# Kernel optimization log

Measured on AMD Instinct MI355X. Metric: run time of the kernel, lower is better.

Reference implementation:

```python
import jax, jax.numpy as jnp
import numpy as np

B, TD, TE, H = 8, 128, 256, 512


def setup_inputs() -> dict:
    key = jax.random.key(0)
    k1, k2, k3, k4, k5, k6 = jax.random.split(key, 6)
    enc = jax.random.normal(k1, (B, TE, H), dtype=jnp.float32)
    dec = jax.random.normal(k2, (B, TD, H), dtype=jnp.float32)
    mask = jax.random.randint(k3, (B, TE), 0, 2).astype(jnp.bool_)
    # glorot-ish scale for weights
    W1 = jax.random.normal(k4, (H, H), dtype=jnp.float32) * (1.0 / np.sqrt(H))
    W2 = jax.random.normal(k5, (H, H), dtype=jnp.float32) * (1.0 / np.sqrt(H))
    V = jax.random.normal(k6, (H, 1), dtype=jnp.float32) * (1.0 / np.sqrt(H))
    return {"encoder_outputs": enc, "decoder_outputs": dec,
            "encoder_mask": mask, "W1": W1, "W2": W2, "V": V}


def reference(encoder_outputs, decoder_outputs, encoder_mask, W1, W2, V):
    # Bahdanau additive attention.
    # enc: [B, Te, H], dec: [B, Td, H], mask: [B, Te]
    ew = jnp.einsum('bsh,hk->bsk', encoder_outputs, W1)   # [B, Te, H]
    dw = jnp.einsum('bth,hk->btk', decoder_outputs, W2)   # [B, Td, H]
    # broadcast add -> [B, Td, Te, H] (the large intermediate)
    s = jnp.tanh(ew[:, None, :, :] + dw[:, :, None, :])
    score = jnp.einsum('btsh,h->bts', s, V[:, 0])          # [B, Td, Te]
    m = encoder_mask.astype(jnp.float32)                   # [B, Te]
    score = score + (1.0 - m)[:, None, :] * (-1e9)
    attention_weights = jax.nn.softmax(score, axis=2)      # [B, Td, Te]
    context_vector = jnp.einsum('bts,bsh->bth', attention_weights, encoder_outputs)
    return context_vector, attention_weights
```

## Files before the change

### kernel.cpp

```cpp
#include <hip/hip_runtime.h>
#include <hip/hip_bf16.h>
#include <math.h>

constexpr int kB  = 8;
constexpr int kTD = 128;
constexpr int kTE = 256;
constexpr int kH  = 512;

constexpr float kTwoLog2e = 2.8853900817779268f;
constexpr float kLog2e    = 1.4426950408889634f;

constexpr int TM = 4;
constexpr int GEMM_BLOCKS = 384;

typedef __attribute__((ext_vector_type(8)))  short short8;
typedef __attribute__((ext_vector_type(16))) float f32x16;

__device__ __forceinline__ unsigned short f2bf(float x) {
    unsigned int u = __float_as_uint(x);
    return (unsigned short)((u + 0x7fffu + ((u >> 16) & 1u)) >> 16);
}
__device__ __forceinline__ float bf2f(unsigned short h) {
    return __uint_as_float(((unsigned int)h) << 16);
}

__global__ __launch_bounds__(256)
void prep_kernel(const float* __restrict__ enc, const float* __restrict__ dec,
                 const float* __restrict__ W1, const float* __restrict__ W2,
                 const void* __restrict__ mask_raw,
                 float* __restrict__ ewt, float* __restrict__ dwc,
                 float* __restrict__ mask_f) {
    const int bx = blockIdx.x;
    const int tid = threadIdx.x;

    if (bx == GEMM_BLOCKS) {
        const unsigned int* w = (const unsigned int*)mask_raw;
        unsigned int gt1 = 0, flt = 0;
        for (int i = tid; i < 512; i += 256) {
            unsigned int v = w[i];
            if (v == 0x3f800000u) flt = 1;
            else if (v > 1u) gt1 = 1;
        }
        __shared__ unsigned int s_gt1, s_flt;
        if (tid == 0) { s_gt1 = 0u; s_flt = 0u; }
        __syncthreads();
        if (gt1) atomicOr(&s_gt1, 1u);
        if (flt) atomicOr(&s_flt, 1u);
        __syncthreads();
        const int mode = s_flt ? 2 : (s_gt1 ? 1 : 0);
        for (int i = tid; i < kB * kTE; i += 256) {
            float val;
            if (mode == 2)      val = ((const float*)mask_raw)[i];
            else if (mode == 1) val = (float)(((const unsigned char*)mask_raw)[i]);
            else                val = (float)(((const int*)mask_raw)[i]);
            mask_f[i] = val;
        }
        return;
    }

    const int mt = bx >> 3;
    const int nt = bx & 7;
    const bool is_enc = (mt < 32);
    const int m0 = mt * 64;
    const int n0 = nt * 64;
    const float* Abase = is_enc ? (enc + (size_t)m0 * kH)
                                : (dec + (size_t)(m0 - 2048) * kH);
    const float* W = is_enc ? W1 : W2;

    __shared__ __align__(16) unsigned short Ahi[64][40], Alo[64][40];
    __shared__ __align__(16) unsigned short Bhi[64][40], Blo[64][40];
    __shared__ float Ws[32][68];

    const int lane = tid & 63;
    const int wv   = tid >> 6;
    const int wr   = wv >> 1, wc = wv & 1;
    const int col  = lane & 31, hi5 = lane >> 5;

    const int ar  = tid >> 2;
    const int akc = (tid & 3) * 8;
    const int wkr = tid >> 3;
    const int wnc = (tid & 7) * 8;
    const int pn  = tid & 63;
    const int pkc = (tid >> 6) * 8;

    f32x16 acc = {};

    float4 a0p = *(const float4*)&Abase[(size_t)ar * kH + akc];
    float4 a1p = *(const float4*)&Abase[(size_t)ar * kH + akc + 4];
    float4 w0p = *(const float4*)&W[(size_t)wkr * kH + n0 + wnc];
    float4 w1p = *(const float4*)&W[(size_t)wkr * kH + n0 + wnc + 4];

    for (int step = 0; step < 16; ++step) {
        *(float4*)&Ws[wkr][wnc]     = w0p;
        *(float4*)&Ws[wkr][wnc + 4] = w1p;
        {
            uint4 H, L;
            float f[8] = {a0p.x, a0p.y, a0p.z, a0p.w, a1p.x, a1p.y, a1p.z, a1p.w};
            unsigned short hs[8], ls[8];
            #pragma unroll
            for (int j = 0; j < 8; ++j) {
                hs[j] = f2bf(f[j]);
                ls[j] = f2bf(f[j] - bf2f(hs[j]));
            }
            H.x = hs[0] | (hs[1] << 16); H.y = hs[2] | (hs[3] << 16);
            H.z = hs[4] | (hs[5] << 16); H.w = hs[6] | (hs[7] << 16);
            L.x = ls[0] | (ls[1] << 16); L.y = ls[2] | (ls[3] << 16);
            L.z = ls[4] | (ls[5] << 16); L.w = ls[6] | (ls[7] << 16);
            *(uint4*)&Ahi[ar][akc] = H;
            *(uint4*)&Alo[ar][akc] = L;
        }
        __syncthreads();

        {
            uint4 H, L;
            unsigned short hs[8], ls[8];
            #pragma unroll
            for (int j = 0; j < 8; ++j) {
                float x = Ws[pkc + j][pn];
                hs[j] = f2bf(x);
                ls[j] = f2bf(x - bf2f(hs[j]));
            }
            H.x = hs[0] | (hs[1] << 16); H.y = hs[2] | (hs[3] << 16);
            H.z = hs[4] | (hs[5] << 16); H.w = hs[6] | (hs[7] << 16);
            L.x = ls[0] | (ls[1] << 16); L.y = ls[2] | (ls[3] << 16);
            L.z = ls[4] | (ls[5] << 16); L.w = ls[6] | (ls[7] << 16);
            *(uint4*)&Bhi[pn][pkc] = H;
            *(uint4*)&Blo[pn][pkc] = L;
        }

        if (step < 15) {
            const int k1 = (step + 1) * 32;
            a0p = *(const float4*)&Abase[(size_t)ar * kH + k1 + akc];
            a1p = *(const float4*)&Abase[(size_t)ar * kH + k1 + akc + 4];
            w0p = *(const float4*)&W[(size_t)(k1 + wkr) * kH + n0 + wnc];
            w1p = *(const float4*)&W[(size_t)(k1 + wkr) * kH + n0 + wnc + 4];
        }
        __syncthreads();

        #pragma unroll
        for (int kc = 0; kc < 32; kc += 16) {
            const int ka = kc + hi5 * 8;
            short8 ah = *(const short8*)&Ahi[wr * 32 + col][ka];
            short8 al = *(const short8*)&Alo[wr * 32 + col][ka];
            short8 bh = *(const short8*)&Bhi[wc * 32 + col][ka];
            short8 bl = *(const short8*)&Blo[wc * 32 + col][ka];
            acc = __builtin_amdgcn_mfma_f32_32x32x16_bf16(ah, bh, acc, 0, 0, 0);
            acc = __builtin_amdgcn_mfma_f32_32x32x16_bf16(ah, bl, acc, 0, 0, 0);
            acc = __builtin_amdgcn_mfma_f32_32x32x16_bf16(al, bh, acc, 0, 0, 0);
        }
        __syncthreads();
    }

    const int h = n0 + wc * 32 + col;
    if (is_enc) {
        #pragma unroll
        for (int reg = 0; reg < 16; ++reg) {
            const int row = (reg & 3) + 8 * (reg >> 2) + 4 * hi5;
            const int gm = m0 + wr * 32 + row;
            const int bb = gm >> 8, sE = gm & 255;
            float val = __builtin_amdgcn_exp2f(acc[reg] * kTwoLog2e);
            ewt[(((size_t)bb * 128 + (h >> 2)) * 256 + sE) * 4 + (h & 3)] = val;
        }
    } else {
        #pragma unroll
        for (int reg = 0; reg < 16; ++reg) {
            const int row = (reg & 3) + 8 * (reg >> 2) + 4 * hi5;
            const int dm = (m0 - 2048) + wr * 32 + row;
            float val = __builtin_amdgcn_exp2f(acc[reg] * kTwoLog2e);
            dwc[(size_t)dm * kH + h] = val;
        }
    }
}

__global__ __launch_bounds__(1024, 4)
void fused_attn_kernel(const float* __restrict__ ewt, const float* __restrict__ dwc,
                       const float* __restrict__ enc, const float* __restrict__ V,
                       const float* __restrict__ mask_f,
                       float* __restrict__ ctx_out, float* __restrict__ attn_out) {
    const int bid  = blockIdx.x;
    const int b    = bid & 7;
    const int t0   = (bid >> 3) * TM;
    const int tid  = threadIdx.x;
    const int lane = tid & 63;
    const int w    = tid >> 6;

    __shared__ float p_s[TM * kH];
    __shared__ float v_s[kH];
    __shared__ union {
        float  F[8 * 1024];
        float4 pctx[4][TM][128];
    } u;
    __shared__ float4 wgt4[kTE];

    if (tid < 512)
        ((float4*)p_s)[tid] =
            ((const float4*)(dwc + (size_t)(b * kTD + t0) * kH))[tid];
    else if (tid < 640)
        ((float4*)v_s)[tid - 512] = ((const float4*)V)[tid - 512];
    __syncthreads();

    const float4* E4b = (const float4*)ewt + (size_t)(b * 128 + w * 8) * 256;
    const float4* Pq  = (const float4*)p_s;
    const float4* Vq  = (const float4*)v_s;

    float acc00=0.f, acc01=0.f, acc02=0.f, acc03=0.f;
    float acc10=0.f, acc11=0.f, acc12=0.f, acc13=0.f;
    float acc20=0.f, acc21=0.f, acc22=0.f, acc23=0.f;
    float acc30=0.f, acc31=0.f, acc32=0.f, acc33=0.f;

#define SCORE_T(eV, qV, accv)                                              \
    {   float A_ = fmaf(eV.x, qV.x, 1.0f), B_ = fmaf(eV.y, qV.y, 1.0f);    \
        float C_ = fmaf(eV.z, qV.z, 1.0f), D_ = fmaf(eV.w, qV.w, 1.0f);    \
        float t1 = fmaf(vv.y, A_, vv.x * B_);                              \
        float t2 = fmaf(vv.w, C_, vv.z * D_);                              \
        float AB = A_ * B_, CD = C_ * D_;                                  \
        float num = fmaf(t2, AB, t1 * CD);                                 \
        accv = fmaf(num, __builtin_amdgcn_rcpf(AB * CD), accv); }
#define SCORE_J(jj)                                                        \
    {   float4 e = E4b[(size_t)hg * 256 + lane + 64 * (jj)];               \
        SCORE_T(e, q0, acc##jj##0) SCORE_T(e, q1, acc##jj##1)              \
        SCORE_T(e, q2, acc##jj##2) SCORE_T(e, q3, acc##jj##3) }

    #pragma unroll 2
    for (int hg = 0; hg < 8; ++hg) {
        const int h4 = w * 8 + hg;
        float4 vv = Vq[h4];
        float4 q0 = Pq[0 * 128 + h4];
        float4 q1 = Pq[1 * 128 + h4];
        float4 q2 = Pq[2 * 128 + h4];
        float4 q3 = Pq[3 * 128 + h4];
        SCORE_J(0) SCORE_J(1) SCORE_J(2) SCORE_J(3)
    }
#undef SCORE_J
#undef SCORE_T

#define WRITE_ACC(dst)                                                     \
    {   dst[0*64]=acc00;  dst[1*64]=acc01;  dst[2*64]=acc02;  dst[3*64]=acc03;  \
        dst[4*64]=acc10;  dst[5*64]=acc11;  dst[6*64]=acc12;  dst[7*64]=acc13;  \
        dst[8*64]=acc20;  dst[9*64]=acc21;  dst[10*64]=acc22; dst[11*64]=acc23; \
        dst[12*64]=acc30; dst[13*64]=acc31; dst[14*64]=acc32; dst[15*64]=acc33; }
#define READ_ACC(src)                                                      \
    {   acc00+=src[0*64];  acc01+=src[1*64];  acc02+=src[2*64];  acc03+=src[3*64];  \
        acc10+=src[4*64];  acc11+=src[5*64];  acc12+=src[6*64];  acc13+=src[7*64];  \
        acc20+=src[8*64];  acc21+=src[9*64];  acc22+=src[10*64]; acc23+=src[11*64]; \
        acc30+=src[12*64]; acc31+=src[13*64]; acc32+=src[14*64]; acc33+=src[15*64]; }

    #pragma unroll
    for (int size = 16; size > 1; size >>= 1) {
        const int half = size >> 1;
        if (w >= half && w < size) {
            float* dst = u.F + (size_t)(w - half) * 1024 + lane;
            WRITE_ACC(dst)
        }
        __syncthreads();
        if (w < half) {
            const float* src = u.F + (size_t)w * 1024 + lane;
            READ_ACC(src)
        }
        __syncthreads();
    }
#undef WRITE_ACC
#undef READ_ACC

    if (w == 0) {
        float pen0 = (1.0f - mask_f[b * kTE + lane +   0]) * -1e9f;
        float pen1 = (1.0f - mask_f[b * kTE + lane +  64]) * -1e9f;
        float pen2 = (1.0f - mask_f[b * kTE + lane + 128]) * -1e9f;
        float pen3 = (1.0f - mask_f[b * kTE + lane + 192]) * -1e9f;
        float sc[4][4];
        sc[0][0] = fmaf(-2.f, acc00, pen0); sc[0][1] = fmaf(-2.f, acc10, pen1);
        sc[0][2] = fmaf(-2.f, acc20, pen2); sc[0][3] = fmaf(-2.f, acc30, pen3);
        sc[1][0] = fmaf(-2.f, acc01, pen0); sc[1][1] = fmaf(-2.f, acc11, pen1);
        sc[1][2] = fmaf(-2.f, acc21, pen2); sc[1][3] = fmaf(-2.f, acc31, pen3);
        sc[2][0] = fmaf(-2.f, acc02, pen0); sc[2][1] = fmaf(-2.f, acc12, pen1);
        sc[2][2] = fmaf(-2.f, acc22, pen2); sc[2][3] = fmaf(-2.f, acc32, pen3);
        sc[3][0] = fmaf(-2.f, acc03, pen0); sc[3][1] = fmaf(-2.f, acc13, pen1);
        sc[3][2] = fmaf(-2.f, acc23, pen2); sc[3][3] = fmaf(-2.f, acc33, pen3);

        #pragma unroll
        for (int t = 0; t < 4; ++t) {
            float m = fmaxf(fmaxf(sc[t][0], sc[t][1]), fmaxf(sc[t][2], sc[t][3]));
            #pragma unroll
            for (int off = 1; off < 64; off <<= 1)
                m = fmaxf(m, __shfl_xor(m, off));
            float pj0 = __builtin_amdgcn_exp2f((sc[t][0] - m) * kLog2e);
            float pj1 = __builtin_amdgcn_exp2f((sc[t][1] - m) * kLog2e);
            float pj2 = __builtin_amdgcn_exp2f((sc[t][2] - m) * kLog2e);
            float pj3 = __builtin_amdgcn_exp2f((sc[t][3] - m) * kLog2e);
            float ssum = (pj0 + pj1) + (pj2 + pj3);
            #pragma unroll
            for (int off = 1; off < 64; off <<= 1)
                ssum += __shfl_xor(ssum, off);
            const float inv = __builtin_amdgcn_rcpf(ssum);
            float* wf = (float*)wgt4;
            float* ao = attn_out + (size_t)(b * kTD + t0 + t) * kTE;
            float g0 = pj0 * inv, g1 = pj1 * inv, g2 = pj2 * inv, g3 = pj3 * inv;
            wf[(lane +   0) * 4 + t] = g0;  ao[lane +   0] = g0;
            wf[(lane +  64) * 4 + t] = g1;  ao[lane +  64] = g1;
            wf[(lane + 128) * 4 + t] = g2;  ao[lane + 128] = g2;
            wf[(lane + 192) * 4 + t] = g3;  ao[lane + 192] = g3;
        }
    }
    __syncthreads();

    const int th4 = tid & 127;
    const int sq  = tid >> 7;
    const float4* enc4 = (const float4*)(enc + (size_t)b * kTE * kH);
    float4 c[TM];
    #pragma unroll
    for (int t = 0; t < TM; ++t) c[t] = float4{0.f, 0.f, 0.f, 0.f};
    #pragma unroll 4
    for (int i = 0; i < 32; ++i) {
        const int ss = sq * 32 + i;
        float4 e = enc4[(size_t)ss * 128 + th4];
        float4 wv = wgt4[ss];
        c[0].x = fmaf(wv.x, e.x, c[0].x); c[0].y = fmaf(wv.x, e.y, c[0].y);
        c[0].z = fmaf(wv.x, e.z, c[0].z); c[0].w = fmaf(wv.x, e.w, c[0].w);
        c[1].x = fmaf(wv.y, e.x, c[1].x); c[1].y = fmaf(wv.y, e.y, c[1].y);
        c[1].z = fmaf(wv.y, e.z, c[1].z); c[1].w = fmaf(wv.y, e.w, c[1].w);
        c[2].x = fmaf(wv.z, e.x, c[2].x); c[2].y = fmaf(wv.z, e.y, c[2].y);
        c[2].z = fmaf(wv.z, e.z, c[2].z); c[2].w = fmaf(wv.z, e.w, c[2].w);
        c[3].x = fmaf(wv.w, e.x, c[3].x); c[3].y = fmaf(wv.w, e.y, c[3].y);
        c[3].z = fmaf(wv.w, e.z, c[3].z); c[3].w = fmaf(wv.w, e.w, c[3].w);
    }
    if (sq >= 4) {
        #pragma unroll
        for (int t = 0; t < TM; ++t) u.pctx[sq - 4][t][th4] = c[t];
    }
    __syncthreads();
    if (sq < 4) {
        #pragma unroll
        for (int t = 0; t < TM; ++t) {
            float4 p = u.pctx[sq][t][th4];
            c[t].x += p.x; c[t].y += p.y; c[t].z += p.z; c[t].w += p.w;
        }
    }
    __syncthreads();
    if (sq >= 1 && sq < 4) {
        #pragma unroll
        for (int t = 0; t < TM; ++t) u.pctx[sq - 1][t][th4] = c[t];
    }
    __syncthreads();
    if (sq == 0) {
        #pragma unroll
        for (int t = 0; t < TM; ++t) {
            float4 q0v = u.pctx[0][t][th4];
            float4 q1v = u.pctx[1][t][th4];
            float4 q2v = u.pctx[2][t][th4];
            c[t].x += (q0v.x + q1v.x) + q2v.x;
            c[t].y += (q0v.y + q1v.y) + q2v.y;
            c[t].z += (q0v.z + q1v.z) + q2v.z;
            c[t].w += (q0v.w + q1v.w) + q2v.w;
            *(float4*)&ctx_out[(size_t)(b * kTD + t0 + t) * kH + th4 * 4] = c[t];
        }
    }
}

extern "C" void kernel_launch(void* const* d_in, const int* in_sizes, int n_in,
                              void* d_out, int out_size, void* d_ws, size_t ws_size,
                              hipStream_t stream) {
    const float* enc  = (const float*)d_in[0];
    const float* dec  = (const float*)d_in[1];
    const void*  mask = d_in[2];
    const float* W1   = (const float*)d_in[3];
    const float* W2   = (const float*)d_in[4];
    const float* V    = (const float*)d_in[5];

    float* ctx_out  = (float*)d_out;
    float* attn_out = (float*)d_out + kB * kTD * kH;

    char* ws = (char*)d_ws;
    float* mask_f = (float*)ws;
    float* ewt    = (float*)(ws + 8192);
    float* dwc    = (float*)(ws + 8192 + (size_t)kB * kTE * kH * 4);

    hipLaunchKernelGGL(prep_kernel, dim3(GEMM_BLOCKS + 1), dim3(256), 0, stream,
                       enc, dec, W1, W2, mask, ewt, dwc, mask_f);
    hipLaunchKernelGGL(fused_attn_kernel, dim3(kB * kTD / TM), dim3(1024), 0, stream,
                       ewt, dwc, enc, V, mask_f, ctx_out, attn_out);
}
```

Measured before the change: 44.77 us.

## Store exp(2*enc·W1) table as bf16 with 8-wide layout and coalesced writes

The encoder projection table (exp of 2x the GEMM output) is now stored as bf16 in 8-element groups instead of fp32 in 4-element groups. The GEMM epilogue stages tiles through a shared-memory union so it can write coalesced 16-byte packets, and block-to-tile mapping is remapped by batch. The attention kernel reads half the bytes for the score loop and unpacks bf16 in registers. The cost is reduced precision of the exp table inside tanh, which may affect accuracy.

```diff
diff --git a/kernel.cpp b/kernel.cpp
--- a/kernel.cpp
+++ b/kernel.cpp
@@ -28,7 +28,7 @@
 void prep_kernel(const float* __restrict__ enc, const float* __restrict__ dec,
                  const float* __restrict__ W1, const float* __restrict__ W2,
                  const void* __restrict__ mask_raw,
-                 float* __restrict__ ewt, float* __restrict__ dwc,
+                 unsigned short* __restrict__ ewt, float* __restrict__ dwc,
                  float* __restrict__ mask_f) {
     const int bx = blockIdx.x;
     const int tid = threadIdx.x;
@@ -58,18 +58,32 @@
         return;
     }
 
-    const int mt = bx >> 3;
-    const int nt = bx & 7;
-    const bool is_enc = (mt < 32);
+    const bool is_enc = (bx < 256);
+    int mt, nt;
+    if (is_enc) {
+        const int bb = bx & 7, j = bx >> 3;
+        mt = bb * 4 + (j & 3);
+        nt = j >> 2;
+    } else {
+        const int b2 = bx - 256;
+        const int bb = b2 & 7, j = b2 >> 3;
+        mt = 32 + bb * 2 + (j & 1);
+        nt = j >> 1;
+    }
     const int m0 = mt * 64;
     const int n0 = nt * 64;
     const float* Abase = is_enc ? (enc + (size_t)m0 * kH)
                                 : (dec + (size_t)(m0 - 2048) * kH);
     const float* W = is_enc ? W1 : W2;
 
-    __shared__ __align__(16) unsigned short Ahi[64][40], Alo[64][40];
-    __shared__ __align__(16) unsigned short Bhi[64][40], Blo[64][40];
-    __shared__ float Ws[32][68];
+    __shared__ __align__(16) union {
+        struct {
+            unsigned short Ahi[64][40], Alo[64][40];
+            unsigned short Bhi[64][40], Blo[64][40];
+            float Ws[32][68];
+        } st;
+        float T[64][68];
+    } sm;
 
     const int lane = tid & 63;
     const int wv   = tid >> 6;
@@ -91,8 +105,8 @@
     float4 w1p = *(const float4*)&W[(size_t)wkr * kH + n0 + wnc + 4];
 
     for (int step = 0; step < 16; ++step) {
-        *(float4*)&Ws[wkr][wnc]     = w0p;
-        *(float4*)&Ws[wkr][wnc + 4] = w1p;
+        *(float4*)&sm.st.Ws[wkr][wnc]     = w0p;
+        *(float4*)&sm.st.Ws[wkr][wnc + 4] = w1p;
         {
             uint4 H, L;
             float f[8] = {a0p.x, a0p.y, a0p.z, a0p.w, a1p.x, a1p.y, a1p.z, a1p.w};
@@ -106,8 +120,8 @@
             H.z = hs[4] | (hs[5] << 16); H.w = hs[6] | (hs[7] << 16);
             L.x = ls[0] | (ls[1] << 16); L.y = ls[2] | (ls[3] << 16);
             L.z = ls[4] | (ls[5] << 16); L.w = ls[6] | (ls[7] << 16);
-            *(uint4*)&Ahi[ar][akc] = H;
-            *(uint4*)&Alo[ar][akc] = L;
+            *(uint4*)&sm.st.Ahi[ar][akc] = H;
+            *(uint4*)&sm.st.Alo[ar][akc] = L;
         }
         __syncthreads();
 
@@ -116,7 +130,7 @@
             unsigned short hs[8], ls[8];
             #pragma unroll
             for (int j = 0; j < 8; ++j) {
-                float x = Ws[pkc + j][pn];
+                float x = sm.st.Ws[pkc + j][pn];
                 hs[j] = f2bf(x);
                 ls[j] = f2bf(x - bf2f(hs[j]));
             }
@@ -124,8 +138,8 @@
             H.z = hs[4] | (hs[5] << 16); H.w = hs[6] | (hs[7] << 16);
             L.x = ls[0] | (ls[1] << 16); L.y = ls[2] | (ls[3] << 16);
             L.z = ls[4] | (ls[5] << 16); L.w = ls[6] | (ls[7] << 16);
-            *(uint4*)&Bhi[pn][pkc] = H;
-            *(uint4*)&Blo[pn][pkc] = L;
+            *(uint4*)&sm.st.Bhi[pn][pkc] = H;
+            *(uint4*)&sm.st.Blo[pn][pkc] = L;
         }
 
         if (step < 15) {
@@ -140,10 +154,10 @@
         #pragma unroll
         for (int kc = 0; kc < 32; kc += 16) {
             const int ka = kc + hi5 * 8;
-            short8 ah = *(const short8*)&Ahi[wr * 32 + col][ka];
-            short8 al = *(const short8*)&Alo[wr * 32 + col][ka];
-            short8 bh = *(const short8*)&Bhi[wc * 32 + col][ka];
-            short8 bl = *(const short8*)&Blo[wc * 32 + col][ka];
+            short8 ah = *(const short8*)&sm.st.Ahi[wr * 32 + col][ka];
+            short8 al = *(const short8*)&sm.st.Alo[wr * 32 + col][ka];
+            short8 bh = *(const short8*)&sm.st.Bhi[wc * 32 + col][ka];
+            short8 bl = *(const short8*)&sm.st.Blo[wc * 32 + col][ka];
             acc = __builtin_amdgcn_mfma_f32_32x32x16_bf16(ah, bh, acc, 0, 0, 0);
             acc = __builtin_amdgcn_mfma_f32_32x32x16_bf16(ah, bl, acc, 0, 0, 0);
             acc = __builtin_amdgcn_mfma_f32_32x32x16_bf16(al, bh, acc, 0, 0, 0);
@@ -151,17 +165,32 @@
         __syncthreads();
     }
 
-    const int h = n0 + wc * 32 + col;
     if (is_enc) {
         #pragma unroll
         for (int reg = 0; reg < 16; ++reg) {
             const int row = (reg & 3) + 8 * (reg >> 2) + 4 * hi5;
-            const int gm = m0 + wr * 32 + row;
-            const int bb = gm >> 8, sE = gm & 255;
-            float val = __builtin_amdgcn_exp2f(acc[reg] * kTwoLog2e);
-            ewt[(((size_t)bb * 128 + (h >> 2)) * 256 + sE) * 4 + (h & 3)] = val;
+            sm.T[wr * 32 + row][wc * 32 + col] =
+                __builtin_amdgcn_exp2f(acc[reg] * kTwoLog2e);
+        }
+        __syncthreads();
+        const int bb  = m0 >> 8;
+        const int sE0 = m0 & 255;
+        uint4* eu = (uint4*)ewt;
+        #pragma unroll
+        for (int i = 0; i < 2; ++i) {
+            const int c   = tid + 256 * i;
+            const int oct = c >> 6;
+            const int sl  = c & 63;
+            const float* tr = &sm.T[sl][oct * 8];
+            uint4 o;
+            o.x = f2bf(tr[0]) | ((unsigned int)f2bf(tr[1]) << 16);
+            o.y = f2bf(tr[2]) | ((unsigned int)f2bf(tr[3]) << 16);
+            o.z = f2bf(tr[4]) | ((unsigned int)f2bf(tr[5]) << 16);
+            o.w = f2bf(tr[6]) | ((unsigned int)f2bf(tr[7]) << 16);
+            eu[((size_t)(bb * 64 + (n0 >> 3) + oct)) * 256 + sE0 + sl] = o;
         }
     } else {
+        const int h = n0 + wc * 32 + col;
         #pragma unroll
         for (int reg = 0; reg < 16; ++reg) {
             const int row = (reg & 3) + 8 * (reg >> 2) + 4 * hi5;
@@ -173,7 +202,8 @@
 }
 
 __global__ __launch_bounds__(1024, 4)
-void fused_attn_kernel(const float* __restrict__ ewt, const float* __restrict__ dwc,
+void fused_attn_kernel(const unsigned short* __restrict__ ewt,
+                       const float* __restrict__ dwc,
                        const float* __restrict__ enc, const float* __restrict__ V,
                        const float* __restrict__ mask_f,
                        float* __restrict__ ctx_out, float* __restrict__ attn_out) {
@@ -199,36 +229,47 @@
         ((float4*)v_s)[tid - 512] = ((const float4*)V)[tid - 512];
     __syncthreads();
 
-    const float4* E4b = (const float4*)ewt + (size_t)(b * 128 + w * 8) * 256;
-    const float4* Pq  = (const float4*)p_s;
-    const float4* Vq  = (const float4*)v_s;
+    const uint4*  E8 = (const uint4*)ewt + ((size_t)(b * 64 + w * 4) * 256 + lane);
+    const float4* Pq = (const float4*)p_s;
+    const float4* Vq = (const float4*)v_s;
 
     float acc00=0.f, acc01=0.f, acc02=0.f, acc03=0.f;
     float acc10=0.f, acc11=0.f, acc12=0.f, acc13=0.f;
     float acc20=0.f, acc21=0.f, acc22=0.f, acc23=0.f;
     float acc30=0.f, acc31=0.f, acc32=0.f, acc33=0.f;
 
-#define SCORE_T(eV, qV, accv)                                              \
-    {   float A_ = fmaf(eV.x, qV.x, 1.0f), B_ = fmaf(eV.y, qV.y, 1.0f);    \
-        float C_ = fmaf(eV.z, qV.z, 1.0f), D_ = fmaf(eV.w, qV.w, 1.0f);    \
-        float t1 = fmaf(vv.y, A_, vv.x * B_);                              \
-        float t2 = fmaf(vv.w, C_, vv.z * D_);                              \
+#define SCORE_T(e4, q4, v4_, accv)                                         \
+    {   float A_ = fmaf(e4.x, q4.x, 1.0f), B_ = fmaf(e4.y, q4.y, 1.0f);    \
+        float C_ = fmaf(e4.z, q4.z, 1.0f), D_ = fmaf(e4.w, q4.w, 1.0f);    \
+        float t1 = fmaf(v4_.y, A_, v4_.x * B_);                            \
+        float t2 = fmaf(v4_.w, C_, v4_.z * D_);                            \
         float AB = A_ * B_, CD = C_ * D_;                                  \
         float num = fmaf(t2, AB, t1 * CD);                                 \
         accv = fmaf(num, __builtin_amdgcn_rcpf(AB * CD), accv); }
 #define SCORE_J(jj)                                                        \
-    {   float4 e = E4b[(size_t)hg * 256 + lane + 64 * (jj)];               \
-        SCORE_T(e, q0, acc##jj##0) SCORE_T(e, q1, acc##jj##1)              \
-        SCORE_T(e, q2, acc##jj##2) SCORE_T(e, q3, acc##jj##3) }
-
-    #pragma unroll 2
-    for (int hg = 0; hg < 8; ++hg) {
-        const int h4 = w * 8 + hg;
-        float4 vv = Vq[h4];
-        float4 q0 = Pq[0 * 128 + h4];
-        float4 q1 = Pq[1 * 128 + h4];
-        float4 q2 = Pq[2 * 128 + h4];
-        float4 q3 = Pq[3 * 128 + h4];
+    {   uint4 eu = E8[(size_t)oct * 256 + 64 * (jj)];                      \
+        float4 ea, eb;                                                     \
+        ea.x = __uint_as_float(eu.x << 16);                                \
+        ea.y = __uint_as_float(eu.x & 0xffff0000u);                        \
+        ea.z = __uint_as_float(eu.y << 16);                                \
+        ea.w = __uint_as_float(eu.y & 0xffff0000u);                        \
+        eb.x = __uint_as_float(eu.z << 16);                                \
+        eb.y = __uint_as_float(eu.z & 0xffff0000u);                        \
+        eb.z = __uint_as_float(eu.w << 16);                                \
+        eb.w = __uint_as_float(eu.w & 0xffff0000u);                        \
+        SCORE_T(ea, q0a, vva, acc##jj##0) SCORE_T(eb, q0b, vvb, acc##jj##0)\
+        SCORE_T(ea, q1a, vva, acc##jj##1) SCORE_T(eb, q1b, vvb, acc##jj##1)\
+        SCORE_T(ea, q2a, vva, acc##jj##2) SCORE_T(eb, q2b, vvb, acc##jj##2)\
+        SCORE_T(ea, q3a, vva, acc##jj##3) SCORE_T(eb, q3b, vvb, acc##jj##3)}
+
+    #pragma unroll
+    for (int oct = 0; oct < 4; ++oct) {
+        const int h4 = w * 8 + oct * 2;
+        float4 vva = Vq[h4],           vvb = Vq[h4 + 1];
+        float4 q0a = Pq[0 * 128 + h4], q0b = Pq[0 * 128 + h4 + 1];
+        float4 q1a = Pq[1 * 128 + h4], q1b = Pq[1 * 128 + h4 + 1];
+        float4 q2a = Pq[2 * 128 + h4], q2b = Pq[2 * 128 + h4 + 1];
+        float4 q3a = Pq[3 * 128 + h4], q3b = Pq[3 * 128 + h4 + 1];
         SCORE_J(0) SCORE_J(1) SCORE_J(2) SCORE_J(3)
     }
 #undef SCORE_J
@@ -370,9 +411,9 @@
     float* attn_out = (float*)d_out + kB * kTD * kH;
 
     char* ws = (char*)d_ws;
-    float* mask_f = (float*)ws;
-    float* ewt    = (float*)(ws + 8192);
-    float* dwc    = (float*)(ws + 8192 + (size_t)kB * kTE * kH * 4);
+    float*          mask_f = (float*)ws;
+    unsigned short* ewt    = (unsigned short*)(ws + 8192);
+    float*          dwc    = (float*)(ws + 8192 + 2097152);
 
     hipLaunchKernelGGL(prep_kernel, dim3(GEMM_BLOCKS + 1), dim3(256), 0, stream,
                        enc, dec, W1, W2, mask, ewt, dwc, mask_f);
```

New measurement: 77.35 us. +72.8%, slower.
